# Kernel tuning notes

Measured on AMD Instinct MI355X. Metric: run time of the kernel, lower is better.

The kernel has to match this reference:

```python
import math
import jax, jax.numpy as jnp
import numpy as np

B, T, C = 2, 2048, 1024
H, Ca = 16, 64


def setup_inputs() -> dict:
    key = jax.random.key(0)
    ks = jax.random.split(key, 5)
    # kaiming-uniform-ish scale for weights
    wb = 1.0 / math.sqrt(C)
    return {
        "x": jax.random.normal(ks[0], (B, T, C), dtype=jnp.float32),
        "w_q": jax.random.uniform(ks[1], (H, C, Ca), jnp.float32, -wb, wb),
        "w_k": jax.random.uniform(ks[2], (H, C, Ca), jnp.float32, -wb, wb),
        "w_v": jax.random.uniform(ks[3], (H, C, Ca), jnp.float32, -wb, wb),
        "w_o": jax.random.uniform(ks[4], (C, C), jnp.float32, -wb, wb),
    }


def reference(x, w_q, w_k, w_v, w_o):
    # x: [B,T,C]; w_q/w_k/w_v: [H,C,Ca]; w_o: [C,C]
    scale = 1.0 / math.sqrt(w_q.shape[-1])
    q = jnp.einsum("btc,hca->bhta", x, w_q)  # [B,H,T,Ca]
    k = jnp.einsum("btc,hca->bhta", x, w_k)
    v = jnp.einsum("btc,hca->bhta", x, w_v)
    s = jnp.einsum("bhta,bhsa->bhts", q, k)  # [B,H,T,T]
    # faithful to original: mask where tril(s)==0, scale applied after masking
    s_hat = jnp.where(jnp.tril(s) == 0, -jnp.inf, s * scale)
    a = jax.nn.softmax(s_hat, axis=-1)
    y = jnp.einsum("bhts,bhsa->bhta", a, v)  # [B,H,T,Ca]
    y_cat = y.transpose(0, 2, 1, 3).reshape(x.shape)  # [B,T,C]
    return y_cat @ w_o
```

## Files before the change

kernel.cpp:

```cpp
#include <hip/hip_runtime.h>
#include <stdint.h>

#define Bc 2
#define Tc 2048
#define Cn 1024
#define Hc 16
#define CAc 64

typedef __attribute__((ext_vector_type(8))) short short8;
typedef __attribute__((ext_vector_type(4))) float f32x4;

__device__ __forceinline__ unsigned short f2bf(float f) {
    unsigned int u = __builtin_bit_cast(unsigned int, f);
    return (unsigned short)((u + 0x7fffu + ((u >> 16) & 1u)) >> 16);
}
__device__ __forceinline__ unsigned int pack_trunc(float a, float b) {
    unsigned int ua = __builtin_bit_cast(unsigned int, a);
    unsigned int ub = __builtin_bit_cast(unsigned int, b);
    return (ua >> 16) | (ub & 0xFFFF0000u);
}

__device__ __forceinline__ void async_cp16(const unsigned short* g, unsigned short* l) {
    __builtin_amdgcn_global_load_lds(
        (const __attribute__((address_space(1))) unsigned int*)g,
        (__attribute__((address_space(3))) unsigned int*)l,
        16, 0, 0);
}

__global__ __launch_bounds__(256) void detect_dtype(
    const unsigned short* __restrict__ x, int* __restrict__ flag)
{
    __shared__ int cnt;
    if (threadIdx.x == 0) cnt = 0;
    __syncthreads();
    int c = 0;
#pragma unroll
    for (int i = 0; i < 8; i++) {
        int idx = (threadIdx.x * 8 + i) * 2;
        unsigned short u = x[idx];
        int e = (u >> 7) & 0xFF;
        if (e >= 0x68 && e <= 0x90) c++;
    }
    atomicAdd(&cnt, c);
    __syncthreads();
    if (threadIdx.x == 0) *flag = (cnt > 1024) ? 1 : 0;
}

__device__ __forceinline__ unsigned short ld_elem(const void* base, size_t off, int isbf) {
    return isbf ? ((const unsigned short*)base)[off] : f2bf(((const float*)base)[off]);
}

__global__ __launch_bounds__(256) void prep(
    const void* __restrict__ xin, unsigned short* __restrict__ xb,
    const void* __restrict__ wq, const void* __restrict__ wk,
    const void* __restrict__ wv, const void* __restrict__ wo,
    unsigned short* __restrict__ wT, unsigned short* __restrict__ woT,
    const int* __restrict__ flag)
{
    const int isbf = *flag;
    const int bx = blockIdx.x;
    if (bx < 4096) {
        int idx = (bx * 256 + threadIdx.x) * 4;
        if (isbf) {
            *(uint2*)(&xb[idx]) = *(const uint2*)((const unsigned short*)xin + idx);
        } else {
            const float* xf = (const float*)xin;
            float4 v = *(const float4*)(xf + idx);
            union { unsigned short s[4]; uint2 u; } p;
            p.s[0] = f2bf(v.x); p.s[1] = f2bf(v.y); p.s[2] = f2bf(v.z); p.s[3] = f2bf(v.w);
            *(uint2*)(&xb[idx]) = p.u;
        }
        return;
    }
    __shared__ unsigned short tile[32][33];
    const int t = threadIdx.x;
    const int tx = t & 31, ty = t >> 5;
    const void* src;
    unsigned short* dst;
    int R, Cw, r0, c0;
    if (bx < 7168) {
        int rem0 = bx - 4096;
        int g = rem0 >> 6;
        int rem = rem0 & 63;
        int ct = rem >> 1;
        int at = rem & 1;
        int proj = g >> 4, h = g & 15;
        const void* wsel = (proj == 0) ? wq : ((proj == 1) ? wk : wv);
        src = isbf ? (const void*)((const unsigned short*)wsel + (size_t)h * Cn * CAc)
                   : (const void*)((const float*)wsel + (size_t)h * Cn * CAc);
        dst = wT + (size_t)g * CAc * Cn;
        R = Cn; Cw = CAc; r0 = ct * 32; c0 = at * 32;
    } else {
        int rem = bx - 7168;
        src = wo; dst = woT;
        R = Cn; Cw = Cn;
        r0 = (rem >> 5) * 32; c0 = (rem & 31) * 32;
    }
#pragma unroll
    for (int j = 0; j < 4; j++)
        tile[ty + j * 8][tx] = ld_elem(src, (size_t)(r0 + ty + j * 8) * Cw + c0 + tx, isbf);
    __syncthreads();
#pragma unroll
    for (int j = 0; j < 4; j++)
        dst[(size_t)(c0 + ty + j * 8) * R + r0 + tx] = tile[tx][ty + j * 8];
}

__global__ __launch_bounds__(256) void gemm_qkv(
    const unsigned short* __restrict__ Amat,
    const unsigned short* __restrict__ Bt,
    unsigned short* __restrict__ o0,
    unsigned short* __restrict__ o1,
    unsigned short* __restrict__ o2)
{
    __shared__ alignas(16) unsigned short Al[2][128 * 32];
    __shared__ alignas(16) unsigned short Bl[2][128 * 32];
    const int tid = threadIdx.x;
    const int wave = tid >> 6, lane = tid & 63;
    const int l15 = lane & 15, quad = lane >> 4;
    const int mBase = blockIdx.y * 128, nBase = blockIdx.x * 128;
    const int mOff = (wave & 1) * 64, nOff = (wave >> 1) * 64;

    const int srow = lane >> 2;
    const int sgc  = (lane & 3) ^ (srow & 3);
    const int sw = (quad ^ (l15 & 3)) * 8;

    f32x4 acc[4][4];
#pragma unroll
    for (int i = 0; i < 4; i++)
#pragma unroll
        for (int j = 0; j < 4; j++)
            acc[i][j] = (f32x4){0.f, 0.f, 0.f, 0.f};

#pragma unroll
    for (int t = 0; t < 2; t++) {
        int rl = wave * 32 + t * 16;
        async_cp16(Amat + (size_t)(mBase + rl + srow) * Cn + sgc * 8, &Al[0][rl * 32]);
        async_cp16(Bt   + (size_t)(nBase + rl + srow) * Cn + sgc * 8, &Bl[0][rl * 32]);
    }
    __syncthreads();

    for (int kk = 0; kk < 32; kk++) {
        const int cur = kk & 1;
        if (kk < 31) {
            const int k1 = (kk + 1) * 32;
#pragma unroll
            for (int t = 0; t < 2; t++) {
                int rl = wave * 32 + t * 16;
                async_cp16(Amat + (size_t)(mBase + rl + srow) * Cn + k1 + sgc * 8, &Al[1 - cur][rl * 32]);
                async_cp16(Bt   + (size_t)(nBase + rl + srow) * Cn + k1 + sgc * 8, &Bl[1 - cur][rl * 32]);
            }
        }
        short8 af[4], bfr[4];
#pragma unroll
        for (int i = 0; i < 4; i++)
            af[i] = *(const short8*)(&Al[cur][(mOff + i * 16 + l15) * 32 + sw]);
#pragma unroll
        for (int j = 0; j < 4; j++)
            bfr[j] = *(const short8*)(&Bl[cur][(nOff + j * 16 + l15) * 32 + sw]);
#pragma unroll
        for (int i = 0; i < 4; i++)
#pragma unroll
            for (int j = 0; j < 4; j++)
                acc[i][j] = __builtin_amdgcn_mfma_f32_16x16x32_bf16(af[i], bfr[j], acc[i][j], 0, 0, 0);
        __syncthreads();
    }

#pragma unroll
    for (int i = 0; i < 4; i++) {
        int m0 = mBase + mOff + i * 16 + quad * 4;
        int b = m0 >> 11, t0 = m0 & (Tc - 1);
#pragma unroll
        for (int j = 0; j < 4; j++) {
            int n = nBase + nOff + j * 16 + l15;
            int proj = n >> 10, h = (n >> 6) & 15, a = n & 63;
            if (proj == 2) {
                union { unsigned short s[4]; uint2 v; } pk;
#pragma unroll
                for (int r = 0; r < 4; r++) pk.s[r] = f2bf(acc[i][j][r]);
                *(uint2*)(&o2[((size_t)(b * Hc + h) * CAc + a) * Tc + t0]) = pk.v;
            } else {
                unsigned short* dst = (proj == 0) ? o0 : o1;
                size_t base = ((size_t)(b * Hc + h) * Tc + t0) * CAc + a;
#pragma unroll
                for (int r = 0; r < 4; r++)
                    dst[base + (size_t)r * CAc] = f2bf(acc[i][j][r]);
            }
        }
    }
}

__global__ __launch_bounds__(256) void gemm_out(
    const unsigned short* __restrict__ Amat,
    const unsigned short* __restrict__ Bt,
    void* __restrict__ o0,
    const int* __restrict__ flag)
{
    __shared__ alignas(16) unsigned short Al[2][64 * 32];
    __shared__ alignas(16) unsigned short Bl[2][128 * 32];
    const int tid = threadIdx.x;
    const int wave = tid >> 6, lane = tid & 63;
    const int l15 = lane & 15, quad = lane >> 4;
    const int mBase = blockIdx.y * 64, nBase = blockIdx.x * 128;
    const int mOff = (wave & 1) * 32, nOff = (wave >> 1) * 64;

    const int srow = lane >> 2;
    const int sgc  = (lane & 3) ^ (srow & 3);
    const int sw = (quad ^ (l15 & 3)) * 8;

    f32x4 acc[2][4];
#pragma unroll
    for (int i = 0; i < 2; i++)
#pragma unroll
        for (int j = 0; j < 4; j++)
            acc[i][j] = (f32x4){0.f, 0.f, 0.f, 0.f};

    {
        int rlA = wave * 16;
        async_cp16(Amat + (size_t)(mBase + rlA + srow) * Cn + sgc * 8, &Al[0][rlA * 32]);
#pragma unroll
        for (int t = 0; t < 2; t++) {
            int rlB = wave * 32 + t * 16;
            async_cp16(Bt + (size_t)(nBase + rlB + srow) * Cn + sgc * 8, &Bl[0][rlB * 32]);
        }
    }
    __syncthreads();

    for (int kk = 0; kk < 32; kk++) {
        const int cur = kk & 1;
        if (kk < 31) {
            const int k1 = (kk + 1) * 32;
            int rlA = wave * 16;
            async_cp16(Amat + (size_t)(mBase + rlA + srow) * Cn + k1 + sgc * 8, &Al[1 - cur][rlA * 32]);
#pragma unroll
            for (int t = 0; t < 2; t++) {
                int rlB = wave * 32 + t * 16;
                async_cp16(Bt + (size_t)(nBase + rlB + srow) * Cn + k1 + sgc * 8, &Bl[1 - cur][rlB * 32]);
            }
        }
        short8 af[2], bfr[4];
#pragma unroll
        for (int i = 0; i < 2; i++)
            af[i] = *(const short8*)(&Al[cur][(mOff + i * 16 + l15) * 32 + sw]);
#pragma unroll
        for (int j = 0; j < 4; j++)
            bfr[j] = *(const short8*)(&Bl[cur][(nOff + j * 16 + l15) * 32 + sw]);
#pragma unroll
        for (int i = 0; i < 2; i++)
#pragma unroll
            for (int j = 0; j < 4; j++)
                acc[i][j] = __builtin_amdgcn_mfma_f32_16x16x32_bf16(af[i], bfr[j], acc[i][j], 0, 0, 0);
        __syncthreads();
    }

    const int isbf = *flag;
#pragma unroll
    for (int i = 0; i < 2; i++) {
        int m0 = mBase + mOff + i * 16 + quad * 4;
#pragma unroll
        for (int j = 0; j < 4; j++) {
            int n = nBase + nOff + j * 16 + l15;
            if (isbf) {
#pragma unroll
                for (int r = 0; r < 4; r++)
                    ((unsigned short*)o0)[(size_t)(m0 + r) * Cn + n] = f2bf(acc[i][j][r]);
            } else {
#pragma unroll
                for (int r = 0; r < 4; r++)
                    ((float*)o0)[(size_t)(m0 + r) * Cn + n] = acc[i][j][r];
            }
        }
    }
}

__global__ __launch_bounds__(256) void attn_pair(
    const unsigned short* __restrict__ q,
    const unsigned short* __restrict__ k,
    const unsigned short* __restrict__ vT,
    unsigned short* __restrict__ y)
{
    __shared__ alignas(16) unsigned short Kl[2][64 * 64];
    __shared__ alignas(16) unsigned short Vl[2][64 * 64];
    const int LDP = 72;
    __shared__ alignas(16) unsigned short Pl[4][16 * LDP];
    const int bx = blockIdx.x;
    const int pr = bx & 15, bh = bx >> 4;
    const int h = bh & 15, b = bh >> 4;
    const int qt1 = pr, qt2 = 31 - pr;
    const int tid = threadIdx.x;
    const int wave = tid >> 6, lane = tid & 63;
    const int l15 = lane & 15, quad = lane >> 4;
    const int m0w1 = qt1 * 64 + wave * 16;
    const int m0w2 = qt2 * 64 + wave * 16;
    const size_t bhoff = (size_t)(b * Hc + h);
    const unsigned short* qh = q + bhoff * Tc * CAc;
    const unsigned short* kh = k + bhoff * Tc * CAc;
    const unsigned short* vh = vT + bhoff * CAc * Tc;

    const int srow = (lane >> 3);
    const int sgc  = (lane & 7) ^ srow;
    const int h7 = l15 & 7;
    const int sw0 = ((quad ^ h7) << 3);
    const int sw1 = (((4 + quad) ^ h7) << 3);

    short8 qf1[2], qf2[2];
#pragma unroll
    for (int s = 0; s < 2; s++) {
        qf1[s] = *(const short8*)(&qh[(size_t)(m0w1 + l15) * CAc + s * 32 + quad * 8]);
        qf2[s] = *(const short8*)(&qh[(size_t)(m0w2 + l15) * CAc + s * 32 + quad * 8]);
    }

    f32x4 oacc1[4], oacc2[4], osum1, osum2;
#pragma unroll
    for (int j2 = 0; j2 < 4; j2++) {
        oacc1[j2] = (f32x4){0.f, 0.f, 0.f, 0.f};
        oacc2[j2] = (f32x4){0.f, 0.f, 0.f, 0.f};
    }
    osum1 = (f32x4){0.f, 0.f, 0.f, 0.f};
    osum2 = (f32x4){0.f, 0.f, 0.f, 0.f};

    const unsigned short ONE = 0x3F80;
    short8 ones;
#pragma unroll
    for (int i = 0; i < 8; i++) ones[i] = (short)ONE;

    unsigned short* Pw = &Pl[wave][0];

#pragma unroll
    for (int t = 0; t < 2; t++) {
        int rl = wave * 16 + t * 8;
        async_cp16(kh + (size_t)(rl + srow) * CAc + sgc * 8, &Kl[0][rl * 64]);
        async_cp16(vh + (size_t)(rl + srow) * Tc  + sgc * 8, &Vl[0][rl * 64]);
    }
    __syncthreads();

    for (int kt = 0; kt <= qt2; kt++) {
        const int k0 = kt * 64;
        const int cur = kt & 1;
        const bool act1 = (kt <= qt1);
        if (kt < qt2) {
            const unsigned short* kg = kh + (size_t)(k0 + 64) * CAc;
            const unsigned short* vg = vh + (k0 + 64);
#pragma unroll
            for (int t = 0; t < 2; t++) {
                int rl = wave * 16 + t * 8;
                async_cp16(kg + (size_t)(rl + srow) * CAc + sgc * 8, &Kl[1 - cur][rl * 64]);
                async_cp16(vg + (size_t)(rl + srow) * Tc  + sgc * 8, &Vl[1 - cur][rl * 64]);
            }
        }
        const unsigned short* Kc = Kl[cur];
        const unsigned short* Vc = Vl[cur];

        float s1[4][4], s2[4][4];
#pragma unroll
        for (int j = 0; j < 4; j++) {
            short8 kf0 = *(const short8*)(&Kc[(j * 16 + l15) * 64 + sw0]);
            short8 kf1 = *(const short8*)(&Kc[(j * 16 + l15) * 64 + sw1]);
            f32x4 z2 = (f32x4){0.f, 0.f, 0.f, 0.f};
            z2 = __builtin_amdgcn_mfma_f32_16x16x32_bf16(kf0, qf2[0], z2, 0, 0, 0);
            z2 = __builtin_amdgcn_mfma_f32_16x16x32_bf16(kf1, qf2[1], z2, 0, 0, 0);
#pragma unroll
            for (int r = 0; r < 4; r++) s2[j][r] = z2[r];
            if (act1) {
                f32x4 z1 = (f32x4){0.f, 0.f, 0.f, 0.f};
                z1 = __builtin_amdgcn_mfma_f32_16x16x32_bf16(kf0, qf1[0], z1, 0, 0, 0);
                z1 = __builtin_amdgcn_mfma_f32_16x16x32_bf16(kf1, qf1[1], z1, 0, 0, 0);
#pragma unroll
                for (int r = 0; r < 4; r++) s1[j][r] = z1[r];
            }
        }

        if (kt == qt2) {
            int tg = m0w2 + l15;
#pragma unroll
            for (int j = 0; j < 4; j++)
#pragma unroll
                for (int r = 0; r < 4; r++) {
                    int sg = k0 + j * 16 + quad * 4 + r;
                    s2[j][r] = (sg <= tg) ? __expf(s2[j][r] * 0.125f) : 0.f;
                }
        } else {
#pragma unroll
            for (int j = 0; j < 4; j++)
#pragma unroll
                for (int r = 0; r < 4; r++)
                    s2[j][r] = __expf(s2[j][r] * 0.125f);
        }
        if (act1) {
            if (kt == qt1) {
                int tg = m0w1 + l15;
#pragma unroll
                for (int j = 0; j < 4; j++)
#pragma unroll
                    for (int r = 0; r < 4; r++) {
                        int sg = k0 + j * 16 + quad * 4 + r;
                        s1[j][r] = (sg <= tg) ? __expf(s1[j][r] * 0.125f) : 0.f;
                    }
            } else {
#pragma unroll
                for (int j = 0; j < 4; j++)
#pragma unroll
                    for (int r = 0; r < 4; r++)
                        s1[j][r] = __expf(s1[j][r] * 0.125f);
            }
        }

        short8 pa2[2], pa1[2];
#pragma unroll
        for (int j = 0; j < 4; j++) {
            uint2 v;
            v.x = pack_trunc(s2[j][0], s2[j][1]);
            v.y = pack_trunc(s2[j][2], s2[j][3]);
            *(uint2*)(&Pw[l15 * LDP + j * 16 + quad * 4]) = v;
        }
#pragma unroll
        for (int c = 0; c < 2; c++)
            pa2[c] = *(const short8*)(&Pw[l15 * LDP + c * 32 + quad * 8]);
        if (act1) {
#pragma unroll
            for (int j = 0; j < 4; j++) {
                uint2 v;
                v.x = pack_trunc(s1[j][0], s1[j][1]);
                v.y = pack_trunc(s1[j][2], s1[j][3]);
                *(uint2*)(&Pw[l15 * LDP + j * 16 + quad * 4]) = v;
            }
#pragma unroll
            for (int c = 0; c < 2; c++)
                pa1[c] = *(const short8*)(&Pw[l15 * LDP + c * 32 + quad * 8]);
        }

#pragma unroll
        for (int c = 0; c < 2; c++) {
#pragma unroll
            for (int j2 = 0; j2 < 4; j2++) {
                short8 vb = *(const short8*)(&Vc[(j2 * 16 + l15) * 64 + (c ? sw1 : sw0)]);
                oacc2[j2] = __builtin_amdgcn_mfma_f32_16x16x32_bf16(pa2[c], vb, oacc2[j2], 0, 0, 0);
                if (act1)
                    oacc1[j2] = __builtin_amdgcn_mfma_f32_16x16x32_bf16(pa1[c], vb, oacc1[j2], 0, 0, 0);
            }
            osum2 = __builtin_amdgcn_mfma_f32_16x16x32_bf16(pa2[c], ones, osum2, 0, 0, 0);
            if (act1)
                osum1 = __builtin_amdgcn_mfma_f32_16x16x32_bf16(pa1[c], ones, osum1, 0, 0, 0);
        }
        __syncthreads();
    }

    float ri1[4], ri2[4];
#pragma unroll
    for (int r = 0; r < 4; r++) { ri1[r] = 1.0f / osum1[r]; ri2[r] = 1.0f / osum2[r]; }
#pragma unroll
    for (int j2 = 0; j2 < 4; j2++) {
#pragma unroll
        for (int r = 0; r < 4; r++) {
            int t1 = m0w1 + quad * 4 + r;
            int t2 = m0w2 + quad * 4 + r;
            y[((size_t)b * Tc + t1) * Cn + h * CAc + j2 * 16 + l15] = f2bf(oacc1[j2][r] * ri1[r]);
            y[((size_t)b * Tc + t2) * Cn + h * CAc + j2 * 16 + l15] = f2bf(oacc2[j2][r] * ri2[r]);
        }
    }
}

extern "C" void kernel_launch(void* const* d_in, const int* in_sizes, int n_in,
                              void* d_out, int out_size, void* d_ws, size_t ws_size,
                              hipStream_t stream) {
    const void* x  = d_in[0];
    const void* wq = d_in[1];
    const void* wk = d_in[2];
    const void* wv = d_in[3];
    const void* wo = d_in[4];
    char* ws = (char*)d_ws;
    int* flag = (int*)(ws);
    unsigned short* wT  = (unsigned short*)(ws + ((size_t)1 << 20));
    unsigned short* woT = (unsigned short*)(ws + ((size_t)7 << 20));
    unsigned short* xb  = (unsigned short*)(ws + ((size_t)9 << 20));
    unsigned short* qb  = (unsigned short*)(ws + ((size_t)17 << 20));
    unsigned short* kb  = (unsigned short*)(ws + ((size_t)25 << 20));
    unsigned short* vTb = (unsigned short*)(ws + ((size_t)33 << 20));
    unsigned short* yb  = (unsigned short*)(ws + ((size_t)41 << 20));

    detect_dtype<<<dim3(1), dim3(256), 0, stream>>>((const unsigned short*)x, flag);
    prep<<<dim3(8192), dim3(256), 0, stream>>>(x, xb, wq, wk, wv, wo, wT, woT, flag);
    gemm_qkv<<<dim3(24, 32), dim3(256), 0, stream>>>(xb, wT, qb, kb, vTb);
    attn_pair<<<dim3(512), dim3(256), 0, stream>>>(qb, kb, vTb, yb);
    gemm_out<<<dim3(8, 64), dim3(256), 0, stream>>>(yb, woT, d_out, flag);
}
```

Measured before the change: 204.0 us.

## Inline dtype detection, fold softmax scale into Q, and stage V transpose through LDS

Removes the separate detect_dtype launch; each kernel now re-detects bf16 by sampling 64 values of x. The bf16 copy of x is skipped when the input is already bf16. The softmax scale times log2(e) is folded into Q during the QKV GEMM epilogue, so attention can use exp2f directly. The transposed V store goes through LDS to produce coalesced 16-byte writes, and pack_trunc now uses a perm instruction. The per-kernel detection adds redundant global reads in every block, and rounding the pre-scaled Q to bf16 changes numerics slightly.

Result: no change. 206.6 us (+1.2%).

```diff
diff --git a/kernel.cpp b/kernel.cpp
--- a/kernel.cpp
+++ b/kernel.cpp
@@ -10,14 +10,18 @@
 typedef __attribute__((ext_vector_type(8))) short short8;
 typedef __attribute__((ext_vector_type(4))) float f32x4;
 
+#define QSCALE 0.18033688011112042f
+
 __device__ __forceinline__ unsigned short f2bf(float f) {
     unsigned int u = __builtin_bit_cast(unsigned int, f);
     return (unsigned short)((u + 0x7fffu + ((u >> 16) & 1u)) >> 16);
 }
+__device__ __forceinline__ unsigned int pack_rne(float a, float b) {
+    return (unsigned int)f2bf(a) | ((unsigned int)f2bf(b) << 16);
+}
 __device__ __forceinline__ unsigned int pack_trunc(float a, float b) {
-    unsigned int ua = __builtin_bit_cast(unsigned int, a);
-    unsigned int ub = __builtin_bit_cast(unsigned int, b);
-    return (ua >> 16) | (ub & 0xFFFF0000u);
+    return __builtin_amdgcn_perm(__builtin_bit_cast(unsigned int, b),
+                                 __builtin_bit_cast(unsigned int, a), 0x07060302u);
 }
 
 __device__ __forceinline__ void async_cp16(const unsigned short* g, unsigned short* l) {
@@ -27,23 +31,15 @@
         16, 0, 0);
 }
 
-__global__ __launch_bounds__(256) void detect_dtype(
-    const unsigned short* __restrict__ x, int* __restrict__ flag)
-{
-    __shared__ int cnt;
-    if (threadIdx.x == 0) cnt = 0;
-    __syncthreads();
+__device__ __forceinline__ int detect_bf16(const unsigned short* x) {
     int c = 0;
 #pragma unroll
-    for (int i = 0; i < 8; i++) {
-        int idx = (threadIdx.x * 8 + i) * 2;
-        unsigned short u = x[idx];
+    for (int i = 0; i < 64; i++) {
+        unsigned short u = x[i * 2];
         int e = (u >> 7) & 0xFF;
-        if (e >= 0x68 && e <= 0x90) c++;
-    }
-    atomicAdd(&cnt, c);
-    __syncthreads();
-    if (threadIdx.x == 0) *flag = (cnt > 1024) ? 1 : 0;
+        c += (e >= 0x68 && e <= 0x90);
+    }
+    return c > 32;
 }
 
 __device__ __forceinline__ unsigned short ld_elem(const void* base, size_t off, int isbf) {
@@ -54,22 +50,19 @@
     const void* __restrict__ xin, unsigned short* __restrict__ xb,
     const void* __restrict__ wq, const void* __restrict__ wk,
     const void* __restrict__ wv, const void* __restrict__ wo,
-    unsigned short* __restrict__ wT, unsigned short* __restrict__ woT,
-    const int* __restrict__ flag)
+    unsigned short* __restrict__ wT, unsigned short* __restrict__ woT)
 {
-    const int isbf = *flag;
+    const int isbf = detect_bf16((const unsigned short*)xin);
     const int bx = blockIdx.x;
     if (bx < 4096) {
+        if (isbf) return;
         int idx = (bx * 256 + threadIdx.x) * 4;
-        if (isbf) {
-            *(uint2*)(&xb[idx]) = *(const uint2*)((const unsigned short*)xin + idx);
-        } else {
-            const float* xf = (const float*)xin;
-            float4 v = *(const float4*)(xf + idx);
-            union { unsigned short s[4]; uint2 u; } p;
-            p.s[0] = f2bf(v.x); p.s[1] = f2bf(v.y); p.s[2] = f2bf(v.z); p.s[3] = f2bf(v.w);
-            *(uint2*)(&xb[idx]) = p.u;
-        }
+        const float* xf = (const float*)xin;
+        float4 v = *(const float4*)(xf + idx);
+        uint2 p;
+        p.x = pack_rne(v.x, v.y);
+        p.y = pack_rne(v.z, v.w);
+        *(uint2*)(&xb[idx]) = p;
         return;
     }
     __shared__ unsigned short tile[32][33];
@@ -106,20 +99,23 @@
 }
 
 __global__ __launch_bounds__(256) void gemm_qkv(
-    const unsigned short* __restrict__ Amat,
+    const void* __restrict__ xin,
+    const unsigned short* __restrict__ xb,
     const unsigned short* __restrict__ Bt,
     unsigned short* __restrict__ o0,
     unsigned short* __restrict__ o1,
     unsigned short* __restrict__ o2)
 {
-    __shared__ alignas(16) unsigned short Al[2][128 * 32];
-    __shared__ alignas(16) unsigned short Bl[2][128 * 32];
+    __shared__ alignas(16) unsigned short SH[4][128 * 32];
     const int tid = threadIdx.x;
     const int wave = tid >> 6, lane = tid & 63;
     const int l15 = lane & 15, quad = lane >> 4;
     const int mBase = blockIdx.y * 128, nBase = blockIdx.x * 128;
     const int mOff = (wave & 1) * 64, nOff = (wave >> 1) * 64;
 
+    const int isbf = detect_bf16((const unsigned short*)xin);
+    const unsigned short* Amat = isbf ? (const unsigned short*)xin : xb;
+
     const int srow = lane >> 2;
     const int sgc  = (lane & 3) ^ (srow & 3);
     const int sw = (quad ^ (l15 & 3)) * 8;
@@ -134,8 +130,8 @@
 #pragma unroll
     for (int t = 0; t < 2; t++) {
         int rl = wave * 32 + t * 16;
-        async_cp16(Amat + (size_t)(mBase + rl + srow) * Cn + sgc * 8, &Al[0][rl * 32]);
-        async_cp16(Bt   + (size_t)(nBase + rl + srow) * Cn + sgc * 8, &Bl[0][rl * 32]);
+        async_cp16(Amat + (size_t)(mBase + rl + srow) * Cn + sgc * 8, &SH[0][rl * 32]);
+        async_cp16(Bt   + (size_t)(nBase + rl + srow) * Cn + sgc * 8, &SH[2][rl * 32]);
     }
     __syncthreads();
 
@@ -146,17 +142,17 @@
 #pragma unroll
             for (int t = 0; t < 2; t++) {
                 int rl = wave * 32 + t * 16;
-                async_cp16(Amat + (size_t)(mBase + rl + srow) * Cn + k1 + sgc * 8, &Al[1 - cur][rl * 32]);
-                async_cp16(Bt   + (size_t)(nBase + rl + srow) * Cn + k1 + sgc * 8, &Bl[1 - cur][rl * 32]);
+                async_cp16(Amat + (size_t)(mBase + rl + srow) * Cn + k1 + sgc * 8, &SH[1 - cur][rl * 32]);
+                async_cp16(Bt   + (size_t)(nBase + rl + srow) * Cn + k1 + sgc * 8, &SH[3 - cur][rl * 32]);
             }
         }
         short8 af[4], bfr[4];
 #pragma unroll
         for (int i = 0; i < 4; i++)
-            af[i] = *(const short8*)(&Al[cur][(mOff + i * 16 + l15) * 32 + sw]);
+            af[i] = *(const short8*)(&SH[cur][(mOff + i * 16 + l15) * 32 + sw]);
 #pragma unroll
         for (int j = 0; j < 4; j++)
-            bfr[j] = *(const short8*)(&Bl[cur][(nOff + j * 16 + l15) * 32 + sw]);
+            bfr[j] = *(const short8*)(&SH[2 + cur][(nOff + j * 16 + l15) * 32 + sw]);
 #pragma unroll
         for (int i = 0; i < 4; i++)
 #pragma unroll
@@ -165,26 +161,51 @@
         __syncthreads();
     }
 
-#pragma unroll
-    for (int i = 0; i < 4; i++) {
-        int m0 = mBase + mOff + i * 16 + quad * 4;
-        int b = m0 >> 11, t0 = m0 & (Tc - 1);
-#pragma unroll
-        for (int j = 0; j < 4; j++) {
-            int n = nBase + nOff + j * 16 + l15;
-            int proj = n >> 10, h = (n >> 6) & 15, a = n & 63;
-            if (proj == 2) {
-                union { unsigned short s[4]; uint2 v; } pk;
-#pragma unroll
-                for (int r = 0; r < 4; r++) pk.s[r] = f2bf(acc[i][j][r]);
-                *(uint2*)(&o2[((size_t)(b * Hc + h) * CAc + a) * Tc + t0]) = pk.v;
-            } else {
-                unsigned short* dst = (proj == 0) ? o0 : o1;
-                size_t base = ((size_t)(b * Hc + h) * Tc + t0) * CAc + a;
+    const int bb = mBase >> 11;
+    if (nBase < 2048) {
+        const float sc = (nBase < 1024) ? QSCALE : 1.0f;
+        unsigned short* dst = (nBase < 1024) ? o0 : o1;
+#pragma unroll
+        for (int i = 0; i < 4; i++) {
+            int m0 = mBase + mOff + i * 16 + quad * 4;
+            int t0 = m0 & (Tc - 1);
+#pragma unroll
+            for (int j = 0; j < 4; j++) {
+                int n = nBase + nOff + j * 16 + l15;
+                int h = (n >> 6) & 15, a = n & 63;
+                size_t base = ((size_t)(bb * Hc + h) * Tc + t0) * CAc + a;
 #pragma unroll
                 for (int r = 0; r < 4; r++)
-                    dst[base + (size_t)r * CAc] = f2bf(acc[i][j][r]);
-            }
+                    dst[base + (size_t)r * CAc] = f2bf(acc[i][j][r] * sc);
+            }
+        }
+    } else {
+        unsigned short* Cl = &SH[0][0];
+#pragma unroll
+        for (int i = 0; i < 4; i++) {
+            int c16 = (mOff >> 3) + i * 2 + (quad >> 1);
+            int p = quad & 1;
+#pragma unroll
+            for (int j = 0; j < 4; j++) {
+                int nl = nOff + j * 16 + l15;
+                int cs = c16 ^ (nl & 7);
+                uint2 v8;
+                v8.x = pack_rne(acc[i][j][0], acc[i][j][1]);
+                v8.y = pack_rne(acc[i][j][2], acc[i][j][3]);
+                *(uint2*)(&Cl[nl * 128 + cs * 8 + p * 4]) = v8;
+            }
+        }
+        __syncthreads();
+        const int tLoc = mBase & (Tc - 1);
+#pragma unroll
+        for (int pp = 0; pp < 8; pp++) {
+            int vr = pp * 16 + wave * 4 + (lane >> 4);
+            int cc = lane & 15;
+            int cs = cc ^ (vr & 7);
+            uint4 val = *(const uint4*)(&Cl[vr * 128 + cs * 8]);
+            int n = nBase + vr;
+            int hh = (n >> 6) & 15, a = n & 63;
+            *(uint4*)(&o2[((size_t)(bb * Hc + hh) * CAc + a) * Tc + tLoc + cc * 8]) = val;
         }
     }
 }
@@ -193,7 +214,7 @@
     const unsigned short* __restrict__ Amat,
     const unsigned short* __restrict__ Bt,
     void* __restrict__ o0,
-    const int* __restrict__ flag)
+    const void* __restrict__ xin)
 {
     __shared__ alignas(16) unsigned short Al[2][64 * 32];
     __shared__ alignas(16) unsigned short Bl[2][128 * 32];
@@ -203,6 +224,8 @@
     const int mBase = blockIdx.y * 64, nBase = blockIdx.x * 128;
     const int mOff = (wave & 1) * 32, nOff = (wave >> 1) * 64;
 
+    const int isbf = detect_bf16((const unsigned short*)xin);
+
     const int srow = lane >> 2;
     const int sgc  = (lane & 3) ^ (srow & 3);
     const int sw = (quad ^ (l15 & 3)) * 8;
@@ -252,7 +275,6 @@
         __syncthreads();
     }
 
-    const int isbf = *flag;
 #pragma unroll
     for (int i = 0; i < 2; i++) {
         int m0 = mBase + mOff + i * 16 + quad * 4;
@@ -376,14 +398,14 @@
 #pragma unroll
                 for (int r = 0; r < 4; r++) {
                     int sg = k0 + j * 16 + quad * 4 + r;
-                    s2[j][r] = (sg <= tg) ? __expf(s2[j][r] * 0.125f) : 0.f;
+                    s2[j][r] = (sg <= tg) ? exp2f(s2[j][r]) : 0.f;
                 }
         } else {
 #pragma unroll
             for (int j = 0; j < 4; j++)
 #pragma unroll
                 for (int r = 0; r < 4; r++)
-                    s2[j][r] = __expf(s2[j][r] * 0.125f);
+                    s2[j][r] = exp2f(s2[j][r]);
         }
         if (act1) {
             if (kt == qt1) {
@@ -393,14 +415,14 @@
 #pragma unroll
                     for (int r = 0; r < 4; r++) {
                         int sg = k0 + j * 16 + quad * 4 + r;
-                        s1[j][r] = (sg <= tg) ? __expf(s1[j][r] * 0.125f) : 0.f;
+                        s1[j][r] = (sg <= tg) ? exp2f(s1[j][r]) : 0.f;
                     }
             } else {
 #pragma unroll
                 for (int j = 0; j < 4; j++)
 #pragma unroll
                     for (int r = 0; r < 4; r++)
-                        s1[j][r] = __expf(s1[j][r] * 0.125f);
+                        s1[j][r] = exp2f(s1[j][r]);
             }
         }
 
@@ -468,7 +490,6 @@
     const void* wv = d_in[3];
     const void* wo = d_in[4];
     char* ws = (char*)d_ws;
-    int* flag = (int*)(ws);
     unsigned short* wT  = (unsigned short*)(ws + ((size_t)1 << 20));
     unsigned short* woT = (unsigned short*)(ws + ((size_t)7 << 20));
     unsigned short* xb  = (unsigned short*)(ws + ((size_t)9 << 20));
@@ -477,9 +498,8 @@
     unsigned short* vTb = (unsigned short*)(ws + ((size_t)33 << 20));
     unsigned short* yb  = (unsigned short*)(ws + ((size_t)41 << 20));
 
-    detect_dtype<<<dim3(1), dim3(256), 0, stream>>>((const unsigned short*)x, flag);
-    prep<<<dim3(8192), dim3(256), 0, stream>>>(x, xb, wq, wk, wv, wo, wT, woT, flag);
-    gemm_qkv<<<dim3(24, 32), dim3(256), 0, stream>>>(xb, wT, qb, kb, vTb);
+    prep<<<dim3(8192), dim3(256), 0, stream>>>(x, xb, wq, wk, wv, wo, wT, woT);
+    gemm_qkv<<<dim3(24, 32), dim3(256), 0, stream>>>(x, xb, wT, qb, kb, vTb);
     attn_pair<<<dim3(512), dim3(256), 0, stream>>>(qb, kb, vTb, yb);
-    gemm_out<<<dim3(8, 64), dim3(256), 0, stream>>>(yb, woT, d_out, flag);
-}
+    gemm_out<<<dim3(8, 64), dim3(256), 0, stream>>>(yb, woT, d_out, x);
+}
```
